# Kernel optimization log

Hardware: AMD Instinct MI355X
Metric: run time of the kernel (lower is better)

The kernel has to match this reference:

```python
import jax, jax.numpy as jnp
import numpy as np

D_MODEL = 1024
NUM_HEADS = 16
HEAD_DIM = D_MODEL // NUM_HEADS


def setup_inputs() -> dict:
    key0 = jax.random.key(0)
    ks = jax.random.split(key0, 11)
    B, S = 8, 4096
    s = 0.02
    return {
        "query": jax.random.normal(ks[0], (B, S, D_MODEL), dtype=jnp.float32),
        "key": jax.random.normal(ks[1], (B, D_MODEL), dtype=jnp.float32),
        "value": jax.random.normal(ks[2], (B, D_MODEL), dtype=jnp.float32),
        "Wq": jax.random.normal(ks[3], (D_MODEL, D_MODEL), dtype=jnp.float32) * s,
        "bq": jnp.zeros((D_MODEL,), dtype=jnp.float32),
        "Wk": jax.random.normal(ks[4], (D_MODEL, HEAD_DIM), dtype=jnp.float32) * s,
        "bk": jnp.zeros((HEAD_DIM,), dtype=jnp.float32),
        "Wv": jax.random.normal(ks[5], (D_MODEL, HEAD_DIM), dtype=jnp.float32) * s,
        "bv": jnp.zeros((HEAD_DIM,), dtype=jnp.float32),
        "Wo": jax.random.normal(ks[6], (D_MODEL, D_MODEL), dtype=jnp.float32) * s,
        "bo": jnp.zeros((D_MODEL,), dtype=jnp.float32),
    }


def reference(query, key, value, Wq, bq, Wk, bk, Wv, bv, Wo, bo):
    B, S, _ = query.shape
    # Q: [B, H, S, hd]
    Q = (query @ Wq + bq).reshape(B, S, NUM_HEADS, HEAD_DIM).transpose(0, 2, 1, 3)
    # shared single K/V vector per batch: [B, hd]
    K = key @ Wk + bk
    V = value @ Wv + bv
    scale = 1.0 / np.sqrt(HEAD_DIM).astype(np.float32)
    # scores: [B, H, S, 1] (kv_len == 1)
    scores = jnp.einsum("bhsd,bd->bhs", Q, K)[..., None] * scale
    attn = jax.nn.softmax(scores, axis=-1)  # softmax over size-1 axis -> ones
    # attended: [B, H, S, hd] = attn * broadcast V
    attended = attn * V[:, None, None, :]
    attended = attended.transpose(0, 2, 1, 3).reshape(B, S, D_MODEL)
    return attended @ Wo + bo
```

## Files before the change

kernel.cpp:

```cpp
#include <hip/hip_runtime.h>


#define D_MODEL 1024
#define HEAD_DIM 64
#define B_SIZE 8
#define S_LEN 4096

typedef float vfloat4 __attribute__((ext_vector_type(4)));

__global__ __launch_bounds__(256) void k_outvec(
    const float* __restrict__ value, const float4* __restrict__ Wv4,
    const float4* __restrict__ bv4, const float* __restrict__ Wo,
    const float* __restrict__ bo, float* __restrict__ outv) {
  int b = blockIdx.x >> 4;
  int jc = blockIdx.x & 15;
  int jbase = jc * 64;
  int t = threadIdx.x;

  __shared__ __align__(16) float Vsh[64];
  {
    int d4 = t & 15;
    int kp = t >> 4;
    const float* vrow = value + b * D_MODEL;
    float4 acc = make_float4(0.f, 0.f, 0.f, 0.f);
    int k0 = kp * 64;
#pragma unroll 8
    for (int i = 0; i < 64; ++i) {
      int k = k0 + i;
      float v = vrow[k];
      float4 w = Wv4[k * 16 + d4];
      acc.x += v * w.x;
      acc.y += v * w.y;
      acc.z += v * w.z;
      acc.w += v * w.w;
    }
    __shared__ float4 red[16][16];
    red[kp][d4] = acc;
    __syncthreads();
    if (t < 16) {
      float4 s = bv4[t];
#pragma unroll
      for (int p = 0; p < 16; ++p) {
        float4 r = red[p][t];
        s.x += r.x;
        s.y += r.y;
        s.z += r.z;
        s.w += r.w;
      }
      ((float4*)Vsh)[t] = s;
    }
    __syncthreads();
  }

  int j = t & 63;
  int part = t >> 6;
  float acc = 0.f;
  int c0 = part * 256;
#pragma unroll 8
  for (int i = 0; i < 256; ++i) {
    int c = c0 + i;
    acc += Vsh[c & 63] * Wo[c * D_MODEL + jbase + j];
  }
  __shared__ float red2[4][64];
  red2[part][j] = acc;
  __syncthreads();
  if (t < 64) {
    outv[b * D_MODEL + jbase + t] =
        red2[0][t] + red2[1][t] + red2[2][t] + red2[3][t] + bo[jbase + t];
  }
}

__global__ __launch_bounds__(256) void k_broadcast(
    const vfloat4* __restrict__ vec4, vfloat4* __restrict__ out4) {
  int b = blockIdx.x >> 7;
  int g = blockIdx.x & 127;
  int t = threadIdx.x;
  vfloat4 v = vec4[b * 256 + t];
  vfloat4* p = out4 + (size_t)b * S_LEN * 256 + (size_t)g * 256 + t;
#pragma unroll 8
  for (int i = 0; i < 32; ++i) {
    __builtin_nontemporal_store(v, p);
    p += 128 * 256;
  }
}

extern "C" void kernel_launch(void* const* d_in, const int* in_sizes, int n_in,
                              void* d_out, int out_size, void* d_ws,
                              size_t ws_size, hipStream_t stream) {
  const float* value = (const float*)d_in[2];
  const float* Wv = (const float*)d_in[7];
  const float* bv = (const float*)d_in[8];
  const float* Wo = (const float*)d_in[9];
  const float* bo = (const float*)d_in[10];

  float* outv = (float*)d_ws;

  k_outvec<<<B_SIZE * 16, 256, 0, stream>>>(value, (const float4*)Wv,
                                            (const float4*)bv, Wo, bo, outv);
  k_broadcast<<<B_SIZE * 128, 256, 0, stream>>>((const vfloat4*)outv,
                                                (vfloat4*)d_out);
}
```

Baseline: 245.7 us.

## Fuse output-vector GEMV and row broadcast into one kernel with float4 Wo loads

Merges the V/Wo projection and the broadcast write into a single kernel, where each block recomputes V, computes a 64-column slice of the output vector with float4 loads of Wo, and then writes that slice across a quarter of the sequence rows. This removes a launch and the workspace round trip, and spreads the GEMV over more blocks. In exchange, V is recomputed redundantly per block and the stores become narrower, strided column slices rather than full contiguous rows.

```diff
diff --git a/kernel.cpp b/kernel.cpp
--- a/kernel.cpp
+++ b/kernel.cpp
@@ -5,16 +5,18 @@
 #define HEAD_DIM 64
 #define B_SIZE 8
 #define S_LEN 4096
+#define ROWGROUPS 4
 
 typedef float vfloat4 __attribute__((ext_vector_type(4)));
 
-__global__ __launch_bounds__(256) void k_outvec(
+__global__ __launch_bounds__(256) void k_fused(
     const float* __restrict__ value, const float4* __restrict__ Wv4,
-    const float4* __restrict__ bv4, const float* __restrict__ Wo,
-    const float* __restrict__ bo, float* __restrict__ outv) {
-  int b = blockIdx.x >> 4;
-  int jc = blockIdx.x & 15;
-  int jbase = jc * 64;
+    const float4* __restrict__ bv4, const float4* __restrict__ Wo4,
+    const float4* __restrict__ bo4, vfloat4* __restrict__ out4) {
+  int blk = blockIdx.x;
+  int b = blk >> 6;
+  int jc = (blk >> 2) & 15;
+  int rg = blk & 3;
   int t = threadIdx.x;
 
   __shared__ __align__(16) float Vsh[64];
@@ -52,35 +54,48 @@
     __syncthreads();
   }
 
-  int j = t & 63;
-  int part = t >> 6;
-  float acc = 0.f;
-  int c0 = part * 256;
+  int j4 = t & 15;
+  int part = t >> 4;
+  int jb4 = jc * 16;
+  __shared__ __align__(16) float slice[64];
+  {
+    float4 acc = make_float4(0.f, 0.f, 0.f, 0.f);
+    int c0 = part * 64;
 #pragma unroll 8
-  for (int i = 0; i < 256; ++i) {
-    int c = c0 + i;
-    acc += Vsh[c & 63] * Wo[c * D_MODEL + jbase + j];
+    for (int i = 0; i < 64; ++i) {
+      int c = c0 + i;
+      float v = Vsh[c & 63];
+      float4 w = Wo4[c * 256 + jb4 + j4];
+      acc.x += v * w.x;
+      acc.y += v * w.y;
+      acc.z += v * w.z;
+      acc.w += v * w.w;
+    }
+    __shared__ float4 red2[16][16];
+    red2[part][j4] = acc;
+    __syncthreads();
+    if (t < 16) {
+      float4 s = bo4[jb4 + t];
+#pragma unroll
+      for (int p = 0; p < 16; ++p) {
+        float4 r = red2[p][t];
+        s.x += r.x;
+        s.y += r.y;
+        s.z += r.z;
+        s.w += r.w;
+      }
+      ((float4*)slice)[t] = s;
+    }
+    __syncthreads();
   }
-  __shared__ float red2[4][64];
-  red2[part][j] = acc;
-  __syncthreads();
-  if (t < 64) {
-    outv[b * D_MODEL + jbase + t] =
-        red2[0][t] + red2[1][t] + red2[2][t] + red2[3][t] + bo[jbase + t];
-  }
-}
 
-__global__ __launch_bounds__(256) void k_broadcast(
-    const vfloat4* __restrict__ vec4, vfloat4* __restrict__ out4) {
-  int b = blockIdx.x >> 7;
-  int g = blockIdx.x & 127;
-  int t = threadIdx.x;
-  vfloat4 v = vec4[b * 256 + t];
-  vfloat4* p = out4 + (size_t)b * S_LEN * 256 + (size_t)g * 256 + t;
+  vfloat4 v = ((const vfloat4*)slice)[j4];
+  int r0 = rg * (S_LEN / ROWGROUPS) + part;
+  vfloat4* p = out4 + (size_t)b * (S_LEN * 256) + (size_t)r0 * 256 + jb4 + j4;
 #pragma unroll 8
-  for (int i = 0; i < 32; ++i) {
+  for (int i = 0; i < 64; ++i) {
     __builtin_nontemporal_store(v, p);
-    p += 128 * 256;
+    p += 16 * 256;
   }
 }
 
@@ -93,10 +108,7 @@
   const float* Wo = (const float*)d_in[9];
   const float* bo = (const float*)d_in[10];
 
-  float* outv = (float*)d_ws;
-
-  k_outvec<<<B_SIZE * 16, 256, 0, stream>>>(value, (const float4*)Wv,
-                                            (const float4*)bv, Wo, bo, outv);
-  k_broadcast<<<B_SIZE * 128, 256, 0, stream>>>((const vfloat4*)outv,
-                                                (vfloat4*)d_out);
+  k_fused<<<B_SIZE * 16 * ROWGROUPS, 256, 0, stream>>>(
+      value, (const float4*)Wv, (const float4*)bv, (const float4*)Wo,
+      (const float4*)bo, (vfloat4*)d_out);
 }
```

Result: no change. 241.1 us (-1.9%).
